# Optimization experiments

Measured on AMD Instinct MI355X. Metric: run time of the kernel, lower is better.

Reference implementation:

```python
import jax, jax.numpy as jnp
import numpy as np

C = 512
HEADS = 8
B, H, W = 2, 64, 64


def setup_inputs() -> dict:
    key = jax.random.key(0)
    k1, k2, k3, k4, k5 = jax.random.split(key, 5)
    s = 1.0 / np.sqrt(C)
    return {
        "hidden_states": jax.random.normal(k1, (B, C, H, W), dtype=jnp.float32),
        "qkv_w": jax.random.normal(k2, (3 * C, C), dtype=jnp.float32) * s,
        "qkv_b": jax.random.normal(k3, (3 * C,), dtype=jnp.float32) * 0.02,
        "proj_w": jax.random.normal(k4, (C, C), dtype=jnp.float32) * s,
        "proj_b": jax.random.normal(k5, (C,), dtype=jnp.float32) * 0.02,
    }


def reference(hidden_states, qkv_w, qkv_b, proj_w, proj_b):
    b, c, h, w = hidden_states.shape
    n = h * w  # sequence length
    heads = HEADS
    dim_head = c // heads
    scale = dim_head ** -0.5

    x = hidden_states.reshape(b, c, n)  # [b, c, n]
    # 1x1 conv1d == matmul over channel dim
    qkv = jnp.einsum("oc,bcn->bon", qkv_w, x) + qkv_b[None, :, None]  # [b, 3c, n]
    q, k, v = jnp.split(qkv, 3, axis=1)
    # [b, heads, dim_head, n] -> [b, heads, n, dim_head]
    def split_heads(t):
        return t.reshape(b, heads, dim_head, n).transpose(0, 1, 3, 2)
    q, k, v = split_heads(q), split_heads(k), split_heads(v)

    attn = jnp.einsum("bhqd,bhkd->bhqk", q, k) * scale  # [b, heads, n, n]
    attn = jax.nn.softmax(attn, axis=-1)
    out = jnp.einsum("bhqk,bhkd->bhqd", attn, v)  # [b, heads, n, dim_head]
    out = out.transpose(0, 1, 3, 2).reshape(b, c, n)  # [b, c, n]
    out = jnp.einsum("oc,bcn->bon", proj_w, out) + proj_b[None, :, None]
    return out  # [b, c, h*w] (matches torch module, no reshape back)
```

## Files before the change

kernel.cpp:

```cpp
#include <hip/hip_runtime.h>


typedef __attribute__((ext_vector_type(8))) short s16x8;
typedef __attribute__((ext_vector_type(4))) float f32x4;
typedef __attribute__((ext_vector_type(16))) float f32x16;
typedef __attribute__((ext_vector_type(4))) unsigned short u16x4;
typedef __attribute__((ext_vector_type(2))) unsigned u32x2;
typedef __attribute__((ext_vector_type(4))) unsigned u32x4;

__device__ __forceinline__ unsigned short f2bf(float f) {
  unsigned u = __builtin_bit_cast(unsigned, f);
  u += 0x7fffu + ((u >> 16) & 1u);
  return (unsigned short)(u >> 16);
}

__device__ __forceinline__ unsigned cvt_pk_bf16(float lo, float hi) {
  unsigned r;
  asm("v_cvt_pk_bf16_f32 %0, %1, %2" : "=v"(r) : "v"(lo), "v"(hi));
  return r;
}

__global__ __launch_bounds__(256) void prep_weights(
    const float* __restrict__ qkv_w, const float* __restrict__ proj_w,
    short* __restrict__ wq, short* __restrict__ wp) {
  int t = blockIdx.x * 256 + threadIdx.x;
  const int NQ = 1536 * 512 / 4;
  if (t < NQ) {
    float4 v = ((const float4*)qkv_w)[t];
    u16x4 o; o[0] = f2bf(v.x); o[1] = f2bf(v.y); o[2] = f2bf(v.z); o[3] = f2bf(v.w);
    ((u16x4*)wq)[t] = o;
  } else {
    int t2 = t - NQ;
    float4 v = ((const float4*)proj_w)[t2];
    u16x4 o; o[0] = f2bf(v.x); o[1] = f2bf(v.y); o[2] = f2bf(v.z); o[3] = f2bf(v.w);
    ((u16x4*)wp)[t2] = o;
  }
}

__global__ __launch_bounds__(256) void prep_transpose(
    const float* __restrict__ x, short* __restrict__ xt) {
  __shared__ short TL[64 * 72];
  const int b = blockIdx.z, c0 = blockIdx.y * 64, n0 = blockIdx.x * 64;
  const int t = threadIdx.x;
  const int cr = t >> 4, n4 = (t & 15) * 4;
#pragma unroll
  for (int i = 0; i < 4; i++) {
    int c = cr + i * 16;
    float4 v = *(const float4*)(x + ((size_t)(b * 512 + c0 + c)) * 4096 + n0 + n4);
    TL[(n4 + 0) * 72 + c] = (short)f2bf(v.x);
    TL[(n4 + 1) * 72 + c] = (short)f2bf(v.y);
    TL[(n4 + 2) * 72 + c] = (short)f2bf(v.z);
    TL[(n4 + 3) * 72 + c] = (short)f2bf(v.w);
  }
  __syncthreads();
  const int n = t >> 2;
#pragma unroll
  for (int s2 = 0; s2 < 2; s2++) {
    int s = (t & 3) * 2 + s2;
    s16x8 v = *(const s16x8*)&TL[n * 72 + s * 8];
    *(s16x8*)(xt + ((size_t)(b * 4096 + n0 + n)) * 512 + c0 + s * 8) = v;
  }
}

__global__ __launch_bounds__(256) void qkv_gemm(
    const short* __restrict__ wq, const short* __restrict__ xt,
    const float* __restrict__ qkv_b,
    short* __restrict__ qkbuf,
    short* __restrict__ vbuf) {
  __shared__ short Al[128 * 40];
  __shared__ short Bl[128 * 40];
  const int b = blockIdx.z;
  const int m0 = blockIdx.y * 128, n0 = blockIdx.x * 128;
  const bool swapped = (blockIdx.y < 8);
  const int t = threadIdx.x, lane = t & 63, wid = t >> 6;
  const int wr = wid >> 1, wc = wid & 1;
  const int srow = t >> 1, scol = (t & 1) * 16;
  const short* gA = wq + (size_t)(m0 + srow) * 512 + scol;
  const short* gB = xt + ((size_t)(b * 4096 + n0 + srow)) * 512 + scol;
  short* lA = &Al[srow * 40 + scol];
  short* lB = &Bl[srow * 40 + scol];
  const short* As = swapped ? Bl : Al;
  const short* Bs = swapped ? Al : Bl;
  f32x4 acc[4][4] = {};
  for (int ks = 0; ks < 16; ks++) {
    *(s16x8*)lA       = *(const s16x8*)(gA + ks * 32);
    *(s16x8*)(lA + 8) = *(const s16x8*)(gA + ks * 32 + 8);
    *(s16x8*)lB       = *(const s16x8*)(gB + ks * 32);
    *(s16x8*)(lB + 8) = *(const s16x8*)(gB + ks * 32 + 8);
    __syncthreads();
    s16x8 af[4], bf[4];
#pragma unroll
    for (int i = 0; i < 4; i++) {
      af[i] = *(const s16x8*)&As[(wr * 64 + i * 16 + (lane & 15)) * 40 + ((lane >> 4) << 3)];
      bf[i] = *(const s16x8*)&Bs[(wc * 64 + i * 16 + (lane & 15)) * 40 + ((lane >> 4) << 3)];
    }
#pragma unroll
    for (int i = 0; i < 4; i++)
#pragma unroll
      for (int j = 0; j < 4; j++)
        acc[i][j] = __builtin_amdgcn_mfma_f32_16x16x32_bf16(af[i], bf[j], acc[i][j], 0, 0, 0);
    __syncthreads();
  }
  if (!swapped) {
#pragma unroll
    for (int i = 0; i < 4; i++)
#pragma unroll
      for (int r = 0; r < 4; r++) {
        int orow = m0 + wr * 64 + i * 16 + ((lane >> 4) << 2) + r;
        float bias = qkv_b[orow];
#pragma unroll
        for (int j = 0; j < 4; j++) {
          int ncol = n0 + wc * 64 + j * 16 + (lane & 15);
          vbuf[((size_t)(b * 512 + orow - 1024)) * 4096 + ncol] = (short)f2bf(acc[i][j][r] + bias);
        }
      }
  } else {
    const float qs = (m0 < 512) ? 0.18033688f : 1.0f;
#pragma unroll
    for (int j = 0; j < 4; j++) {
      int ocol = m0 + wc * 64 + j * 16 + (lane & 15);
      float bias = qkv_b[ocol];
#pragma unroll
      for (int i = 0; i < 4; i++)
#pragma unroll
        for (int r = 0; r < 4; r++) {
          int nrow = n0 + wr * 64 + i * 16 + ((lane >> 4) << 2) + r;
          qkbuf[((size_t)(b * 4096 + nrow)) * 1024 + ocol] = (short)f2bf((acc[i][j][r] + bias) * qs);
        }
    }
  }
}

__global__ __launch_bounds__(256) void flash_attn(
    const short* __restrict__ qkbuf, const short* __restrict__ vbuf,
    short* __restrict__ aout) {
  __shared__ short Kl[64 * 64];
  __shared__ short Vl[64 * 64];
  const int t = threadIdx.x, lane = t & 63, wid = t >> 6;
  const int hi = lane >> 5, q32 = lane & 31;
  const int j = blockIdx.x;
  const int lid = ((j & 7) << 6) + (j >> 3);
  const int qb = (lid & 31) * 128 + wid * 32;
  const int bh = lid >> 5, b = bh >> 3, h = bh & 7;

  s16x8 qf[4];
  {
    const short* qrow = qkbuf + ((size_t)(b * 4096 + qb + q32)) * 1024 + h * 64 + hi * 8;
#pragma unroll
    for (int dc = 0; dc < 4; dc++) qf[dc] = *(const s16x8*)(qrow + dc * 16);
  }

  f32x16 oacc[2] = {};
  float m = -__builtin_inff();
  float l = 0.f;

  const int srow = t >> 2;
  const int swz = (srow & 7) << 4;
  const int o0 = ((t & 3) * 32) ^ swz;
  const int o1 = ((t & 3) * 32 + 16) ^ swz;
  const short* gK = qkbuf + ((size_t)(b * 4096 + srow)) * 1024 + 512 + h * 64 + (t & 3) * 16;
  const short* gV = vbuf + ((size_t)(b * 512 + h * 64 + srow)) * 4096 + (t & 3) * 16;
  char* lKrow = (char*)&Kl[srow * 64];
  char* lVrow = (char*)&Vl[srow * 64];

  s16x8 pk0 = *(const s16x8*)gK, pk1 = *(const s16x8*)(gK + 8);
  s16x8 pv0 = *(const s16x8*)gV, pv1 = *(const s16x8*)(gV + 8);

  for (int kt = 0; kt < 64; kt++) {
    *(s16x8*)(lKrow + o0) = pk0;  *(s16x8*)(lKrow + o1) = pk1;
    *(s16x8*)(lVrow + o0) = pv0;  *(s16x8*)(lVrow + o1) = pv1;
    __syncthreads();
    if (kt < 63) {
      const short* nK = gK + (size_t)(kt + 1) * 64 * 1024;
      const short* nV = gV + (kt + 1) * 64;
      pk0 = *(const s16x8*)nK;  pk1 = *(const s16x8*)(nK + 8);
      pv0 = *(const s16x8*)nV;  pv1 = *(const s16x8*)(nV + 8);
    }
#pragma unroll
    for (int kb = 0; kb < 2; kb++) {
      f32x16 st = {};
      const int krow = kb * 32 + q32;
      const int ksw = (krow & 7) << 4;
#pragma unroll
      for (int dc = 0; dc < 4; dc++) {
        s16x8 kf = *(const s16x8*)((char*)&Kl[krow * 64] + ((dc * 32 + hi * 16) ^ ksw));
        st = __builtin_amdgcn_mfma_f32_32x32x16_bf16(kf, qf[dc], st, 0, 0, 0);
      }
      float tm = st[0];
#pragma unroll
      for (int r2 = 1; r2 < 16; r2++) tm = fmaxf(tm, st[r2]);
      tm = fmaxf(tm, __shfl_xor(tm, 32));
      if (!__all(tm <= m + 8.f)) {
        float mn = fmaxf(m, tm);
        float alpha = exp2f(m - mn);
        m = mn;
        l *= alpha;
#pragma unroll
        for (int di = 0; di < 2; di++)
#pragma unroll
          for (int r2 = 0; r2 < 16; r2++) oacc[di][r2] *= alpha;
      }
      float p[16];
      float ps = 0.f;
#pragma unroll
      for (int r2 = 0; r2 < 16; r2++) { p[r2] = exp2f(st[r2] - m); ps += p[r2]; }
      l += ps;
#pragma unroll
      for (int kh = 0; kh < 2; kh++) {
        unsigned A  = cvt_pk_bf16(p[kh * 8 + 0], p[kh * 8 + 1]);
        unsigned Bu = cvt_pk_bf16(p[kh * 8 + 4], p[kh * 8 + 5]);
        unsigned C  = cvt_pk_bf16(p[kh * 8 + 2], p[kh * 8 + 3]);
        unsigned D  = cvt_pk_bf16(p[kh * 8 + 6], p[kh * 8 + 7]);
        u32x2 r0 = __builtin_amdgcn_permlane32_swap(A, Bu, false, false);
        u32x2 r1 = __builtin_amdgcn_permlane32_swap(C, D, false, false);
        u32x4 uu; uu[0] = r0[0]; uu[1] = r1[0]; uu[2] = r0[1]; uu[3] = r1[1];
        s16x8 pf = __builtin_bit_cast(s16x8, uu);
#pragma unroll
        for (int di = 0; di < 2; di++) {
          const int vrow = di * 32 + q32;
          s16x8 vf = *(const s16x8*)((char*)&Vl[vrow * 64]
                       + ((kb * 64 + kh * 32 + hi * 16) ^ ((vrow & 7) << 4)));
          oacc[di] = __builtin_amdgcn_mfma_f32_32x32x16_bf16(vf, pf, oacc[di], 0, 0, 0);
        }
      }
    }
    __syncthreads();
  }
  l += __shfl_xor(l, 32);
  float inv = 1.f / l;
  short* orow = aout + ((size_t)(b * 4096 + qb + q32)) * 512 + h * 64;
#pragma unroll
  for (int di = 0; di < 2; di++)
#pragma unroll
    for (int blk = 0; blk < 4; blk++) {
      uint2 w;
      w.x = cvt_pk_bf16(oacc[di][blk * 4 + 0] * inv, oacc[di][blk * 4 + 1] * inv);
      w.y = cvt_pk_bf16(oacc[di][blk * 4 + 2] * inv, oacc[di][blk * 4 + 3] * inv);
      *(uint2*)(orow + di * 32 + blk * 8 + hi * 4) = w;
    }
}

__global__ __launch_bounds__(256) void proj_gemm(
    const short* __restrict__ wp, const short* __restrict__ aout,
    const float* __restrict__ proj_b, float* __restrict__ out) {
  __shared__ short Al[128 * 40];
  __shared__ short Bl[128 * 40];
  const int b = blockIdx.z;
  const int m0 = blockIdx.y * 128, n0 = blockIdx.x * 128;
  const int t = threadIdx.x, lane = t & 63, wid = t >> 6;
  const int wr = wid >> 1, wc = wid & 1;
  const int srow = t >> 1, scol = (t & 1) * 16;
  const short* gA = wp + (size_t)(m0 + srow) * 512 + scol;
  const short* gB = aout + ((size_t)(b * 4096 + n0 + srow)) * 512 + scol;
  short* lA = &Al[srow * 40 + scol];
  short* lB = &Bl[srow * 40 + scol];
  f32x4 acc[4][4] = {};
  for (int ks = 0; ks < 16; ks++) {
    *(s16x8*)lA       = *(const s16x8*)(gA + ks * 32);
    *(s16x8*)(lA + 8) = *(const s16x8*)(gA + ks * 32 + 8);
    *(s16x8*)lB       = *(const s16x8*)(gB + ks * 32);
    *(s16x8*)(lB + 8) = *(const s16x8*)(gB + ks * 32 + 8);
    __syncthreads();
    s16x8 af[4], bf[4];
#pragma unroll
    for (int i = 0; i < 4; i++) {
      af[i] = *(const s16x8*)&Al[(wr * 64 + i * 16 + (lane & 15)) * 40 + ((lane >> 4) << 3)];
      bf[i] = *(const s16x8*)&Bl[(wc * 64 + i * 16 + (lane & 15)) * 40 + ((lane >> 4) << 3)];
    }
#pragma unroll
    for (int i = 0; i < 4; i++)
#pragma unroll
      for (int j = 0; j < 4; j++)
        acc[i][j] = __builtin_amdgcn_mfma_f32_16x16x32_bf16(af[i], bf[j], acc[i][j], 0, 0, 0);
    __syncthreads();
  }
#pragma unroll
  for (int i = 0; i < 4; i++)
#pragma unroll
    for (int r = 0; r < 4; r++) {
      int orow = m0 + wr * 64 + i * 16 + ((lane >> 4) << 2) + r;
      float bias = proj_b[orow];
#pragma unroll
      for (int j = 0; j < 4; j++) {
        int ncol = n0 + wc * 64 + j * 16 + (lane & 15);
        out[((size_t)(b * 512 + orow)) * 4096 + ncol] = acc[i][j][r] + bias;
      }
    }
}

extern "C" void kernel_launch(void* const* d_in, const int* in_sizes, int n_in,
                              void* d_out, int out_size, void* d_ws, size_t ws_size,
                              hipStream_t stream) {
  const float* x      = (const float*)d_in[0];
  const float* qkv_w  = (const float*)d_in[1];
  const float* qkv_b  = (const float*)d_in[2];
  const float* proj_w = (const float*)d_in[3];
  const float* proj_b = (const float*)d_in[4];
  float* out = (float*)d_out;
  char* ws = (char*)d_ws;
  short* wq = (short*)(ws);
  short* wp = (short*)(ws + 1572864);
  short* xt = (short*)(ws + 2097152);
  short* qk = (short*)(ws + 10485760);
  short* vb = (short*)(ws + 27262976);
  short* ao = (short*)(ws + 35651584);

  prep_weights  <<<1024, 256, 0, stream>>>(qkv_w, proj_w, wq, wp);
  prep_transpose<<<dim3(64, 8, 2), 256, 0, stream>>>(x, xt);
  qkv_gemm      <<<dim3(32, 12, 2), 256, 0, stream>>>(wq, xt, qkv_b, qk, vb);
  flash_attn    <<<512, 256, 0, stream>>>(qk, vb, ao);
  proj_gemm     <<<dim3(32, 4, 2), 256, 0, stream>>>(wp, ao, proj_b, out);
}
```

Measured before the change: 265.7 us.

## Split flash attention over two KV halves and merge partial results

```diff
diff --git a/kernel.cpp b/kernel.cpp
--- a/kernel.cpp
+++ b/kernel.cpp
@@ -12,6 +12,10 @@
   unsigned u = __builtin_bit_cast(unsigned, f);
   u += 0x7fffu + ((u >> 16) & 1u);
   return (unsigned short)(u >> 16);
+}
+
+__device__ __forceinline__ float bf2f(short s) {
+  return __builtin_bit_cast(float, ((unsigned)(unsigned short)s) << 16);
 }
 
 __device__ __forceinline__ unsigned cvt_pk_bf16(float lo, float hi) {
@@ -133,15 +137,19 @@
 
 __global__ __launch_bounds__(256) void flash_attn(
     const short* __restrict__ qkbuf, const short* __restrict__ vbuf,
-    short* __restrict__ aout) {
+    short* __restrict__ opart,
+    float* __restrict__ mlbuf) {
   __shared__ short Kl[64 * 64];
   __shared__ short Vl[64 * 64];
   const int t = threadIdx.x, lane = t & 63, wid = t >> 6;
   const int hi = lane >> 5, q32 = lane & 31;
   const int j = blockIdx.x;
-  const int lid = ((j & 7) << 6) + (j >> 3);
-  const int qb = (lid & 31) * 128 + wid * 32;
-  const int bh = lid >> 5, b = bh >> 3, h = bh & 7;
+  const int lid = ((j & 7) << 7) + (j >> 3);
+  const int bh = lid >> 6, b = bh >> 3, h = bh & 7;
+  const int rest = lid & 63;
+  const int qc = rest >> 1, half = rest & 1;
+  const int qb = qc * 128 + wid * 32;
+  const int kt0 = half * 32;
 
   s16x8 qf[4];
   {
@@ -158,19 +166,19 @@
   const int swz = (srow & 7) << 4;
   const int o0 = ((t & 3) * 32) ^ swz;
   const int o1 = ((t & 3) * 32 + 16) ^ swz;
-  const short* gK = qkbuf + ((size_t)(b * 4096 + srow)) * 1024 + 512 + h * 64 + (t & 3) * 16;
-  const short* gV = vbuf + ((size_t)(b * 512 + h * 64 + srow)) * 4096 + (t & 3) * 16;
+  const short* gK = qkbuf + ((size_t)(b * 4096 + kt0 * 64 + srow)) * 1024 + 512 + h * 64 + (t & 3) * 16;
+  const short* gV = vbuf + ((size_t)(b * 512 + h * 64 + srow)) * 4096 + kt0 * 64 + (t & 3) * 16;
   char* lKrow = (char*)&Kl[srow * 64];
   char* lVrow = (char*)&Vl[srow * 64];
 
   s16x8 pk0 = *(const s16x8*)gK, pk1 = *(const s16x8*)(gK + 8);
   s16x8 pv0 = *(const s16x8*)gV, pv1 = *(const s16x8*)(gV + 8);
 
-  for (int kt = 0; kt < 64; kt++) {
+  for (int kt = 0; kt < 32; kt++) {
     *(s16x8*)(lKrow + o0) = pk0;  *(s16x8*)(lKrow + o1) = pk1;
     *(s16x8*)(lVrow + o0) = pv0;  *(s16x8*)(lVrow + o1) = pv1;
     __syncthreads();
-    if (kt < 63) {
+    if (kt < 31) {
       const short* nK = gK + (size_t)(kt + 1) * 64 * 1024;
       const short* nV = gV + (kt + 1) * 64;
       pk0 = *(const s16x8*)nK;  pk1 = *(const s16x8*)(nK + 8);
@@ -186,9 +194,13 @@
         s16x8 kf = *(const s16x8*)((char*)&Kl[krow * 64] + ((dc * 32 + hi * 16) ^ ksw));
         st = __builtin_amdgcn_mfma_f32_32x32x16_bf16(kf, qf[dc], st, 0, 0, 0);
       }
-      float tm = st[0];
-#pragma unroll
-      for (int r2 = 1; r2 < 16; r2++) tm = fmaxf(tm, st[r2]);
+      float x0 = fmaxf(st[0], st[1]),  x1 = fmaxf(st[2], st[3]);
+      float x2 = fmaxf(st[4], st[5]),  x3 = fmaxf(st[6], st[7]);
+      float x4 = fmaxf(st[8], st[9]),  x5 = fmaxf(st[10], st[11]);
+      float x6 = fmaxf(st[12], st[13]), x7 = fmaxf(st[14], st[15]);
+      x0 = fmaxf(x0, x1); x2 = fmaxf(x2, x3); x4 = fmaxf(x4, x5); x6 = fmaxf(x6, x7);
+      x0 = fmaxf(x0, x2); x4 = fmaxf(x4, x6);
+      float tm = fmaxf(x0, x4);
       tm = fmaxf(tm, __shfl_xor(tm, 32));
       if (!__all(tm <= m + 8.f)) {
         float mn = fmaxf(m, tm);
@@ -227,17 +239,47 @@
     __syncthreads();
   }
   l += __shfl_xor(l, 32);
-  float inv = 1.f / l;
-  short* orow = aout + ((size_t)(b * 4096 + qb + q32)) * 512 + h * 64;
+  const size_t prow = ((size_t)(half * 16 + bh) * 4096 + qb + q32) * 64;
 #pragma unroll
   for (int di = 0; di < 2; di++)
 #pragma unroll
     for (int blk = 0; blk < 4; blk++) {
       uint2 w;
-      w.x = cvt_pk_bf16(oacc[di][blk * 4 + 0] * inv, oacc[di][blk * 4 + 1] * inv);
-      w.y = cvt_pk_bf16(oacc[di][blk * 4 + 2] * inv, oacc[di][blk * 4 + 3] * inv);
-      *(uint2*)(orow + di * 32 + blk * 8 + hi * 4) = w;
-    }
+      w.x = cvt_pk_bf16(oacc[di][blk * 4 + 0], oacc[di][blk * 4 + 1]);
+      w.y = cvt_pk_bf16(oacc[di][blk * 4 + 2], oacc[di][blk * 4 + 3]);
+      *(uint2*)(opart + prow + di * 32 + blk * 8 + hi * 4) = w;
+    }
+  if (hi == 0) {
+    const size_t mrow = (size_t)(half * 16 + bh) * 4096 + qb + q32;
+    ((float2*)mlbuf)[mrow] = make_float2(m, l);
+  }
+}
+
+__global__ __launch_bounds__(256) void merge_halves(
+    const short* __restrict__ opart, const float* __restrict__ mlbuf,
+    short* __restrict__ aout) {
+  const int row = blockIdx.x * 256 + threadIdx.x;
+  const int bh = row >> 12, q = row & 4095, b = bh >> 3, h = bh & 7;
+  float2 ml0 = ((const float2*)mlbuf)[row];
+  float2 ml1 = ((const float2*)mlbuf)[65536 + row];
+  float mm = fmaxf(ml0.x, ml1.x);
+  float w0 = exp2f(ml0.x - mm), w1 = exp2f(ml1.x - mm);
+  float inv = 1.f / (w0 * ml0.y + w1 * ml1.y);
+  w0 *= inv; w1 *= inv;
+  const s16x8* r0 = (const s16x8*)(opart + (size_t)row * 64);
+  const s16x8* r1 = (const s16x8*)(opart + ((size_t)65536 + row) * 64);
+  short* po = aout + ((size_t)(b * 4096 + q)) * 512 + h * 64;
+#pragma unroll
+  for (int sg = 0; sg < 8; sg++) {
+    s16x8 a0 = r0[sg], a1 = r1[sg];
+    float v[8];
+#pragma unroll
+    for (int i = 0; i < 8; i++) v[i] = w0 * bf2f(a0[i]) + w1 * bf2f(a1[i]);
+    u32x4 uu;
+#pragma unroll
+    for (int k = 0; k < 4; k++) uu[k] = cvt_pk_bf16(v[2 * k], v[2 * k + 1]);
+    *(s16x8*)(po + sg * 8) = __builtin_bit_cast(s16x8, uu);
+  }
 }
 
 __global__ __launch_bounds__(256) void proj_gemm(
@@ -304,10 +346,13 @@
   short* qk = (short*)(ws + 10485760);
   short* vb = (short*)(ws + 27262976);
   short* ao = (short*)(ws + 35651584);
+  short* op = (short*)(ws + 44040192);
+  float* ml = (float*)(ws + 60817408);
 
   prep_weights  <<<1024, 256, 0, stream>>>(qkv_w, proj_w, wq, wp);
   prep_transpose<<<dim3(64, 8, 2), 256, 0, stream>>>(x, xt);
   qkv_gemm      <<<dim3(32, 12, 2), 256, 0, stream>>>(wq, xt, qkv_b, qk, vb);
-  flash_attn    <<<512, 256, 0, stream>>>(qk, vb, ao);
+  flash_attn    <<<1024, 256, 0, stream>>>(qk, vb, op, ml);
+  merge_halves  <<<256, 256, 0, stream>>>(op, ml, ao);
   proj_gemm     <<<dim3(32, 4, 2), 256, 0, stream>>>(wp, ao, proj_b, out);
 }
```

Result: no change. 262.0 us (-1.4%).
